# Kernel tuning notes

Measured on AMD Instinct MI355X. Metric: run time of the kernel, lower is better.

## Reference

```python
import jax, jax.numpy as jnp
import numpy as np

N_NODES = 500_000
N_EDGES = 16_000_000
N_COLORS = 64


def _mix(v, c1, c2):
    """32-bit integer hash (lowbias32-style avalanche mix)."""
    v = v.astype(jnp.uint32)
    v = (v ^ (v >> 16)) * jnp.uint32(c1)
    v = (v ^ (v >> 13)) * jnp.uint32(c2)
    return v ^ (v >> 16)


def setup_inputs() -> dict:
    key = jax.random.key(0)
    k1, k2 = jax.random.split(key)
    x = jax.random.randint(k1, (N_NODES,), 0, N_COLORS, dtype=jnp.int32)
    edge_index = jax.random.randint(k2, (2, N_EDGES), 0, N_NODES, dtype=jnp.int32)
    return {"x": x, "edge_index": edge_index}


def reference(x, edge_index):
    """One Weisfeiler-Lehman color-refinement step.

    Faithful semantics of WLConvOptimized.forward: each node's new label is
    determined by the equivalence class of (own label, multiset of incoming
    neighbor labels). Instead of Python tuple-sort + hash()+dict, we use a
    permutation-invariant multiset hash (sum of two independent 32-bit hashes
    of neighbor labels, combined with the node's own label hash) and then a
    sort-based dense relabeling. Nodes get equal output labels iff their
    (label, neighbor-multiset) signatures collide -- same partition as the
    original (up to astronomically unlikely hash collisions); label numbering
    is canonical (sorted-signature order) rather than dict-insertion order.
    """
    num_nodes = x.shape[0]
    row, col = edge_index[0], edge_index[1]  # message flows row (src) -> col (dst)

    # two independent per-label hashes
    ha = _mix(x, 0x045D9F3B, 0x045D9F3B)
    hb = _mix(x, 0x9E3779B1, 0x85EBCA77)

    # permutation-invariant multiset hash of incoming neighbor labels (gather + scatter-add)
    sum_a = jnp.zeros(num_nodes, jnp.uint32).at[col].add(ha[row])
    sum_b = jnp.zeros(num_nodes, jnp.uint32).at[col].add(hb[row])

    # combine own label with neighbor multiset, re-avalanche
    sig_a = _mix(ha * jnp.uint32(0x27D4EB2F) + sum_a, 0xC2B2AE3D, 0x165667B1)
    sig_b = _mix(hb * jnp.uint32(0x61C88647) + sum_b, 0x045D9F3B, 0x27D4EB2F)

    # dense relabel: sort by (sig_a, sig_b), number distinct signatures 0..K-1
    order = jnp.lexsort((sig_b, sig_a))
    sa, sb = sig_a[order], sig_b[order]
    new_grp = jnp.concatenate([
        jnp.zeros(1, jnp.int32),
        ((sa[1:] != sa[:-1]) | (sb[1:] != sb[:-1])).astype(jnp.int32),
    ])
    labels_sorted = jnp.cumsum(new_grp).astype(jnp.int32)
    out = jnp.zeros(num_nodes, jnp.int32).at[order].set(labels_sorted)
    return out
```

## Files before the change

### kernel.cpp

```cpp
#include <hip/hip_runtime.h>
#include <stdint.h>

#define LOG_B 17
#define NB (1u << LOG_B)
#define FINE_NODES 1024
#define NBKT 512
#define CSH 10
#define EPB 16384
#define ITERS (EPB / 4 / 256)

__host__ __device__ constexpr uint32_t cmix(uint32_t v, uint32_t c1, uint32_t c2) {
    v = (v ^ (v >> 16)) * c1;
    v = (v ^ (v >> 13)) * c2;
    return v ^ (v >> 16);
}

__device__ __forceinline__ uint32_t mixh(uint32_t v, uint32_t c1, uint32_t c2) {
    v = (v ^ (v >> 16)) * c1;
    v = (v ^ (v >> 13)) * c2;
    return v ^ (v >> 16);
}

struct Luts { uint32_t ha[64]; uint32_t hb[64]; };
constexpr Luts make_luts() {
    Luts l{};
    for (uint32_t i = 0; i < 64; i++) {
        l.ha[i] = cmix(i, 0x045D9F3Bu, 0x045D9F3Bu);
        l.hb[i] = cmix(i, 0x9E3779B1u, 0x85EBCA77u);
    }
    return l;
}
__constant__ Luts LUT = make_luts();

__global__ __launch_bounds__(256) void k_pre(const int4* __restrict__ x4,
                                             uchar4* __restrict__ xc4, int n4) {
    int i = blockIdx.x * 256 + threadIdx.x;
    if (i >= n4) return;
    int4 v = x4[i];
    xc4[i] = make_uchar4((uint8_t)v.x, (uint8_t)v.y, (uint8_t)v.z, (uint8_t)v.w);
}

__global__ __launch_bounds__(256, 4) void k_bin(const int* __restrict__ row, const int* __restrict__ col,
                                                const uint8_t* __restrict__ xc, uint16_t* __restrict__ bins,
                                                uint32_t* __restrict__ cursor, int E, int cap) {
    __shared__ uint16_t stage[EPB];
    __shared__ uint32_t hist[NBKT];
    __shared__ uint16_t gb16[NBKT];
    __shared__ uint32_t wsum[4];
    int t = threadIdx.x;
    int lane = t & 63, wid = t >> 6;
    int base = blockIdx.x * EPB;
    int nend = min(E - base, EPB);
    for (int b = t; b < NBKT; b += 256) hist[b] = 0;
    __syncthreads();

    const int4* col4 = (const int4*)(col + base);
    const int4* row4 = (const int4*)(row + base);

    bool fast = (nend == EPB);
    uint32_t rec[ITERS * 4];

    if (fast) {
#pragma unroll
        for (int it = 0; it < ITERS; ++it) {
            int k = t + it * 256;
            int4 c = col4[k];
            int4 r = row4[k];
            atomicAdd(&hist[(uint32_t)c.x >> CSH], 1u);
            atomicAdd(&hist[(uint32_t)c.y >> CSH], 1u);
            atomicAdd(&hist[(uint32_t)c.z >> CSH], 1u);
            atomicAdd(&hist[(uint32_t)c.w >> CSH], 1u);
            rec[it * 4 + 0] = ((uint32_t)c.x << 6) | (uint32_t)xc[r.x];
            rec[it * 4 + 1] = ((uint32_t)c.y << 6) | (uint32_t)xc[r.y];
            rec[it * 4 + 2] = ((uint32_t)c.z << 6) | (uint32_t)xc[r.z];
            rec[it * 4 + 3] = ((uint32_t)c.w << 6) | (uint32_t)xc[r.w];
        }
    } else {
        int n4 = nend >> 2;
        for (int k = t; k < n4; k += 256) {
            int4 c = col4[k];
            atomicAdd(&hist[(uint32_t)c.x >> CSH], 1u);
            atomicAdd(&hist[(uint32_t)c.y >> CSH], 1u);
            atomicAdd(&hist[(uint32_t)c.z >> CSH], 1u);
            atomicAdd(&hist[(uint32_t)c.w >> CSH], 1u);
        }
        for (int k = (n4 << 2) + t; k < nend; k += 256)
            atomicAdd(&hist[(uint32_t)col[base + k] >> CSH], 1u);
    }
    __syncthreads();

    int b0 = 2 * t;
    uint32_t h0 = hist[b0], h1 = hist[b0 + 1];
    uint32_t s = h0 + h1;
    uint32_t inc = s;
    for (int off = 1; off < 64; off <<= 1) {
        uint32_t nv = __shfl_up(inc, (unsigned)off, 64);
        if (lane >= off) inc += nv;
    }
    if (lane == 63) wsum[wid] = inc;
    __syncthreads();
    uint32_t woff = 0;
    for (int w = 0; w < wid; w++) woff += wsum[w];
    uint32_t e0 = woff + inc - s;
    uint32_t g0 = h0 ? atomicAdd(&cursor[b0], h0) : 0u;
    uint32_t g1 = h1 ? atomicAdd(&cursor[b0 + 1], h1) : 0u;
    gb16[b0] = (uint16_t)g0;
    gb16[b0 + 1] = (uint16_t)g1;
    hist[b0] = e0 << 16;
    hist[b0 + 1] = (e0 + h0) << 16;
    __syncthreads();

    if (fast) {
#pragma unroll
        for (int it = 0; it < ITERS * 4; ++it) {
            uint32_t rv = rec[it];
            uint32_t b = rv >> 16;
            uint32_t o = atomicAdd(&hist[b], 1u);
            stage[(o >> 16) + (o & 0xFFFFu)] = (uint16_t)rv;
        }
    } else {
        int n4 = nend >> 2;
        for (int k = t; k < n4; k += 256) {
            int4 c = col4[k];
            int4 r = row4[k];
            {
                uint32_t d = (uint32_t)c.x, b = d >> CSH;
                uint32_t o = atomicAdd(&hist[b], 1u);
                stage[(o >> 16) + (o & 0xFFFFu)] = (uint16_t)(((d & 1023u) << 6) | (uint32_t)xc[r.x]);
            }
            {
                uint32_t d = (uint32_t)c.y, b = d >> CSH;
                uint32_t o = atomicAdd(&hist[b], 1u);
                stage[(o >> 16) + (o & 0xFFFFu)] = (uint16_t)(((d & 1023u) << 6) | (uint32_t)xc[r.y]);
            }
            {
                uint32_t d = (uint32_t)c.z, b = d >> CSH;
                uint32_t o = atomicAdd(&hist[b], 1u);
                stage[(o >> 16) + (o & 0xFFFFu)] = (uint16_t)(((d & 1023u) << 6) | (uint32_t)xc[r.z]);
            }
            {
                uint32_t d = (uint32_t)c.w, b = d >> CSH;
                uint32_t o = atomicAdd(&hist[b], 1u);
                stage[(o >> 16) + (o & 0xFFFFu)] = (uint16_t)(((d & 1023u) << 6) | (uint32_t)xc[r.w]);
            }
        }
        for (int k = (n4 << 2) + t; k < nend; k += 256) {
            int i = base + k;
            uint32_t d = (uint32_t)col[i], b = d >> CSH;
            uint32_t o = atomicAdd(&hist[b], 1u);
            stage[(o >> 16) + (o & 0xFFFFu)] = (uint16_t)(((d & 1023u) << 6) | (uint32_t)xc[row[i]]);
        }
    }
    __syncthreads();

    int sub = lane >> 4, l16 = lane & 15;
    for (int b = wid * 4 + sub; b < NBKT; b += 16) {
        uint32_t hv = hist[b];
        uint32_t cnt = hv & 0xFFFFu;
        if (!cnt) continue;
        uint32_t s0 = hv >> 16;
        uint16_t* dst = bins + (size_t)b * (uint32_t)cap + gb16[b];
        for (uint32_t off = l16; off < cnt; off += 16)
            dst[off] = stage[s0 + off];
    }
}

__global__ __launch_bounds__(1024) void k_accsig(const uint16_t* __restrict__ bins,
                                                 const uint32_t* __restrict__ cursor,
                                                 const uint8_t* __restrict__ xc,
                                                 unsigned long long* __restrict__ sigs,
                                                 uint32_t* __restrict__ bcnt, int N, int cap) {
    __shared__ uint32_t sA[FINE_NODES];
    __shared__ uint32_t sB[FINE_NODES];
    __shared__ uint32_t lA[64], lB[64];
    int t = threadIdx.x;
    int b = blockIdx.x;
    sA[t] = 0;
    sB[t] = 0;
    if (t < 64) { lA[t] = LUT.ha[t]; lB[t] = LUT.hb[t]; }
    __syncthreads();

    uint32_t m = cursor[b];
    const uint16_t* mybins = bins + (size_t)b * (uint32_t)cap;
    const uint2* p16v = (const uint2*)mybins;
    uint32_t m4 = m >> 2;
    for (uint32_t k = t; k < m4; k += 1024) {
        uint2 rv = p16v[k];
        {
            uint32_t rec = rv.x & 0xFFFFu, n = rec >> 6, c = rec & 63u;
            atomicAdd(&sA[n], lA[c]);
            atomicAdd(&sB[n], lB[c]);
        }
        {
            uint32_t rec = rv.x >> 16, n = rec >> 6, c = rec & 63u;
            atomicAdd(&sA[n], lA[c]);
            atomicAdd(&sB[n], lB[c]);
        }
        {
            uint32_t rec = rv.y & 0xFFFFu, n = rec >> 6, c = rec & 63u;
            atomicAdd(&sA[n], lA[c]);
            atomicAdd(&sB[n], lB[c]);
        }
        {
            uint32_t rec = rv.y >> 16, n = rec >> 6, c = rec & 63u;
            atomicAdd(&sA[n], lA[c]);
            atomicAdd(&sB[n], lB[c]);
        }
    }
    for (uint32_t k = (m4 << 2) + t; k < m; k += 1024) {
        uint32_t rec = mybins[k], n = rec >> 6, c = rec & 63u;
        atomicAdd(&sA[n], lA[c]);
        atomicAdd(&sB[n], lB[c]);
    }
    __syncthreads();

    int g = b * FINE_NODES + t;
    if (g < N) {
        uint32_t xv = (uint32_t)xc[g];
        uint32_t ha = lA[xv];
        uint32_t hb = lB[xv];
        uint32_t sa = mixh(ha * 0x27D4EB2Fu + sA[t], 0xC2B2AE3Du, 0x165667B1u);
        uint32_t sb = mixh(hb * 0x61C88647u + sB[t], 0x045D9F3Bu, 0x27D4EB2Fu);
        unsigned long long key = ((unsigned long long)sa << 32) | (unsigned long long)sb;
        sigs[g] = key;
        atomicAdd(&bcnt[(uint32_t)(key >> (64 - LOG_B))], 1u);
    }
}

__global__ __launch_bounds__(256) void k_scan1(const uint32_t* __restrict__ in,
                                               uint32_t* __restrict__ out,
                                               uint32_t* __restrict__ part) {
    __shared__ uint32_t wsum[4];
    int t = threadIdx.x;
    int lane = t & 63, wid = t >> 6;
    int base = blockIdx.x * 1024 + 4 * t;
    uint4 v = *(const uint4*)(in + base);
    uint32_t s = v.x + v.y + v.z + v.w;
    uint32_t inc = s;
    for (int off = 1; off < 64; off <<= 1) {
        uint32_t nv = __shfl_up(inc, (unsigned)off, 64);
        if (lane >= off) inc += nv;
    }
    if (lane == 63) wsum[wid] = inc;
    __syncthreads();
    uint32_t woff = 0;
    for (int w = 0; w < wid; w++) woff += wsum[w];
    uint32_t e = woff + inc - s;
    uint4 o;
    o.x = e; o.y = e + v.x; o.z = o.y + v.y; o.w = o.z + v.z;
    *(uint4*)(out + base) = o;
    if (t == 255) part[blockIdx.x] = wsum[0] + wsum[1] + wsum[2] + wsum[3];
}

__global__ void k_scan2(uint32_t* __restrict__ part) {
    __shared__ uint32_t s[256];
    int t = threadIdx.x;
    uint32_t v = part[t];
    s[t] = v;
    __syncthreads();
    for (int off = 1; off < 256; off <<= 1) {
        uint32_t add = (t >= off) ? s[t - off] : 0u;
        __syncthreads();
        s[t] += add;
        __syncthreads();
    }
    part[t] = s[t] - v;
}

__global__ __launch_bounds__(256) void k_scan3(uint32_t* __restrict__ out,
                                               const uint32_t* __restrict__ part) {
    int base = blockIdx.x * 1024 + 4 * threadIdx.x;
    uint32_t p = part[blockIdx.x];
    uint4 v = *(const uint4*)(out + base);
    v.x += p; v.y += p; v.z += p; v.w += p;
    *(uint4*)(out + base) = v;
}

__global__ void k_scatter(const unsigned long long* __restrict__ sigs,
                          const uint32_t* __restrict__ boff, uint32_t* __restrict__ bcur,
                          unsigned long long* __restrict__ skey, uint32_t* __restrict__ snode,
                          int N) {
    int i = blockIdx.x * blockDim.x + threadIdx.x;
    if (i >= N) return;
    unsigned long long key = sigs[i];
    uint32_t b = (uint32_t)(key >> (64 - LOG_B));
    uint32_t pos = boff[b] + atomicAdd(&bcur[b], 1u);
    skey[pos] = key;
    snode[pos] = (uint32_t)i;
}

__global__ void k_bsort(unsigned long long* __restrict__ skey, uint32_t* __restrict__ snode,
                        const uint32_t* __restrict__ boff, uint32_t* __restrict__ ldx,
                        uint32_t* __restrict__ dcnt, int N) {
    int b = blockIdx.x * blockDim.x + threadIdx.x;
    if (b >= (int)NB) return;
    uint32_t s0 = boff[b];
    uint32_t s1 = (b == (int)NB - 1) ? (uint32_t)N : boff[b + 1];
    for (uint32_t i = s0 + 1; i < s1; i++) {
        unsigned long long k = skey[i];
        uint32_t nd = snode[i];
        uint32_t j = i;
        while (j > s0 && skey[j - 1] > k) {
            skey[j] = skey[j - 1];
            snode[j] = snode[j - 1];
            j--;
        }
        skey[j] = k;
        snode[j] = nd;
    }
    uint32_t d = 0;
    unsigned long long prev = 0ull;
    for (uint32_t i = s0; i < s1; i++) {
        unsigned long long k = skey[i];
        if (i == s0 || k != prev) d++;
        prev = k;
        ldx[i] = d - 1;
    }
    dcnt[b] = d;
}

__global__ void k_out(const unsigned long long* __restrict__ skey,
                      const uint32_t* __restrict__ snode, const uint32_t* __restrict__ ldx,
                      const uint32_t* __restrict__ doff, int* __restrict__ out, int N) {
    int i = blockIdx.x * blockDim.x + threadIdx.x;
    if (i >= N) return;
    unsigned long long key = skey[i];
    uint32_t b = (uint32_t)(key >> (64 - LOG_B));
    out[snode[i]] = (int)(doff[b] + ldx[i]);
}

extern "C" void kernel_launch(void* const* d_in, const int* in_sizes, int n_in,
                              void* d_out, int out_size, void* d_ws, size_t ws_size,
                              hipStream_t stream) {
    const int* x = (const int*)d_in[0];
    const int* ei = (const int*)d_in[1];
    int N = in_sizes[0];
    int E = in_sizes[1] / 2;
    const int* row = ei;
    const int* col = ei + E;

    int nacc = (N + FINE_NODES - 1) / FINE_NODES;
    int cap = E / NBKT + (E / NBKT) / 16 + 1024;
    cap = (cap + 3) & ~3;

    char* p = (char*)d_ws;
    auto alloc = [&](size_t bytes) -> char* {
        char* r = p;
        p += (bytes + 255) & ~(size_t)255;
        return r;
    };
    uint32_t* cursor = (uint32_t*)alloc((size_t)NBKT * 4);
    uint32_t* bcnt   = (uint32_t*)alloc((size_t)NB * 4);
    uint32_t* bcur   = (uint32_t*)alloc((size_t)NB * 4);
    uint32_t* dcnt   = (uint32_t*)alloc((size_t)NB * 4);
    uint32_t* part   = (uint32_t*)alloc(256 * 4);
    size_t zbytes = (size_t)(p - (char*)d_ws);
    uint8_t* xc = (uint8_t*)alloc((size_t)N);
    unsigned long long* sigs = (unsigned long long*)alloc((size_t)N * 8);
    uint16_t* bins = (uint16_t*)alloc((size_t)NBKT * cap * 2);
    char* q = (char*)bins;
    auto alias = [&](size_t bytes) -> char* {
        char* r = q;
        q += (bytes + 255) & ~(size_t)255;
        return r;
    };
    unsigned long long* skey = (unsigned long long*)alias((size_t)N * 8);
    uint32_t* snode = (uint32_t*)alias((size_t)N * 4);
    uint32_t* ldx   = (uint32_t*)alias((size_t)N * 4);
    uint32_t* boff  = (uint32_t*)alias((size_t)NB * 4);
    uint32_t* doff  = (uint32_t*)alias((size_t)NB * 4);

    hipMemsetAsync(d_ws, 0, zbytes, stream);

    int nbN = (N + 255) / 256;
    int nbBin = (E + EPB - 1) / EPB;
    int n4 = N / 4;

    k_pre<<<(n4 + 255) / 256, 256, 0, stream>>>((const int4*)x, (uchar4*)xc, n4);
    k_bin<<<nbBin, 256, 0, stream>>>(row, col, xc, bins, cursor, E, cap);
    k_accsig<<<nacc, 1024, 0, stream>>>(bins, cursor, xc, sigs, bcnt, N, cap);

    k_scan1<<<NB / 1024, 256, 0, stream>>>(bcnt, boff, part);
    k_scan2<<<1, 256, 0, stream>>>(part);
    k_scan3<<<NB / 1024, 256, 0, stream>>>(boff, part);

    k_scatter<<<nbN, 256, 0, stream>>>(sigs, boff, bcur, skey, snode, N);
    k_bsort<<<NB / 256, 256, 0, stream>>>(skey, snode, boff, ldx, dcnt, N);

    k_scan1<<<NB / 1024, 256, 0, stream>>>(dcnt, doff, part);
    k_scan2<<<1, 256, 0, stream>>>(part);
    k_scan3<<<NB / 1024, 256, 0, stream>>>(doff, part);

    k_out<<<nbN, 256, 0, stream>>>(skey, snode, ldx, doff, (int*)d_out, N);
}
```

Measured before the change: 397.9 us.

## Fuse scan, scatter, bucket sort and output into one cooperative kernel

Replaces the chain of eight small kernels (two three-pass scans, scatter, bucket sort, output) with a single cooperative kernel of 512 blocks that uses grid-wide syncs between phases. This is meant to remove per-launch overhead and the idle gaps between dependent launches in the tail. The cost is many grid.sync barriers, a cooperative-launch residency requirement, and one block doing the partial-sum scan serially while the other blocks wait.

```diff
diff --git a/kernel.cpp b/kernel.cpp
--- a/kernel.cpp
+++ b/kernel.cpp
@@ -1,5 +1,8 @@
 #include <hip/hip_runtime.h>
+#include <hip/hip_cooperative_groups.h>
 #include <stdint.h>
+
+namespace cg = cooperative_groups;
 
 #define LOG_B 17
 #define NB (1u << LOG_B)
@@ -227,106 +230,110 @@
     }
 }
 
-__global__ __launch_bounds__(256) void k_scan1(const uint32_t* __restrict__ in,
-                                               uint32_t* __restrict__ out,
-                                               uint32_t* __restrict__ part) {
-    __shared__ uint32_t wsum[4];
+
+__device__ __forceinline__ void scan_nb(const uint32_t* __restrict__ in,
+                                        uint32_t* __restrict__ outp,
+                                        uint32_t* __restrict__ part,
+                                        uint32_t* sh, uint32_t* shw,
+                                        cg::grid_group& grid) {
     int t = threadIdx.x;
     int lane = t & 63, wid = t >> 6;
-    int base = blockIdx.x * 1024 + 4 * t;
-    uint4 v = *(const uint4*)(in + base);
-    uint32_t s = v.x + v.y + v.z + v.w;
-    uint32_t inc = s;
+    int g = blockIdx.x * 256 + t;
+    uint32_t v = in[g];
+    uint32_t inc = v;
     for (int off = 1; off < 64; off <<= 1) {
         uint32_t nv = __shfl_up(inc, (unsigned)off, 64);
         if (lane >= off) inc += nv;
     }
-    if (lane == 63) wsum[wid] = inc;
+    if (lane == 63) shw[wid] = inc;
     __syncthreads();
     uint32_t woff = 0;
-    for (int w = 0; w < wid; w++) woff += wsum[w];
-    uint32_t e = woff + inc - s;
-    uint4 o;
-    o.x = e; o.y = e + v.x; o.z = o.y + v.y; o.w = o.z + v.z;
-    *(uint4*)(out + base) = o;
-    if (t == 255) part[blockIdx.x] = wsum[0] + wsum[1] + wsum[2] + wsum[3];
-}
-
-__global__ void k_scan2(uint32_t* __restrict__ part) {
-    __shared__ uint32_t s[256];
+    for (int w = 0; w < wid; w++) woff += shw[w];
+    uint32_t excl = woff + inc - v;
+    if (t == 255) part[blockIdx.x] = woff + inc;
+    grid.sync();
+    if (blockIdx.x == 0) {
+        uint32_t o0 = part[t], o1 = part[t + 256];
+        sh[t] = o0; sh[t + 256] = o1;
+        __syncthreads();
+        for (int off = 1; off < 512; off <<= 1) {
+            uint32_t a0 = (t >= off) ? sh[t - off] : 0u;
+            uint32_t a1 = (t + 256 >= off) ? sh[t + 256 - off] : 0u;
+            __syncthreads();
+            sh[t] += a0; sh[t + 256] += a1;
+            __syncthreads();
+        }
+        part[t] = sh[t] - o0;
+        part[t + 256] = sh[t + 256] - o1;
+    }
+    grid.sync();
+    outp[g] = excl + part[blockIdx.x];
+}
+
+__global__ __launch_bounds__(256) void k_tail(const unsigned long long* __restrict__ sigs,
+                                              const uint32_t* __restrict__ bcnt,
+                                              uint32_t* __restrict__ boff,
+                                              uint32_t* __restrict__ bcur,
+                                              unsigned long long* __restrict__ skey,
+                                              uint32_t* __restrict__ snode,
+                                              uint32_t* __restrict__ ldx,
+                                              uint32_t* __restrict__ dcnt,
+                                              uint32_t* __restrict__ doff,
+                                              uint32_t* __restrict__ part,
+                                              int* __restrict__ out, int N) {
+    cg::grid_group grid = cg::this_grid();
+    __shared__ uint32_t sh[512];
+    __shared__ uint32_t shw[4];
     int t = threadIdx.x;
-    uint32_t v = part[t];
-    s[t] = v;
-    __syncthreads();
-    for (int off = 1; off < 256; off <<= 1) {
-        uint32_t add = (t >= off) ? s[t - off] : 0u;
-        __syncthreads();
-        s[t] += add;
-        __syncthreads();
-    }
-    part[t] = s[t] - v;
-}
-
-__global__ __launch_bounds__(256) void k_scan3(uint32_t* __restrict__ out,
-                                               const uint32_t* __restrict__ part) {
-    int base = blockIdx.x * 1024 + 4 * threadIdx.x;
-    uint32_t p = part[blockIdx.x];
-    uint4 v = *(const uint4*)(out + base);
-    v.x += p; v.y += p; v.z += p; v.w += p;
-    *(uint4*)(out + base) = v;
-}
-
-__global__ void k_scatter(const unsigned long long* __restrict__ sigs,
-                          const uint32_t* __restrict__ boff, uint32_t* __restrict__ bcur,
-                          unsigned long long* __restrict__ skey, uint32_t* __restrict__ snode,
-                          int N) {
-    int i = blockIdx.x * blockDim.x + threadIdx.x;
-    if (i >= N) return;
-    unsigned long long key = sigs[i];
-    uint32_t b = (uint32_t)(key >> (64 - LOG_B));
-    uint32_t pos = boff[b] + atomicAdd(&bcur[b], 1u);
-    skey[pos] = key;
-    snode[pos] = (uint32_t)i;
-}
-
-__global__ void k_bsort(unsigned long long* __restrict__ skey, uint32_t* __restrict__ snode,
-                        const uint32_t* __restrict__ boff, uint32_t* __restrict__ ldx,
-                        uint32_t* __restrict__ dcnt, int N) {
-    int b = blockIdx.x * blockDim.x + threadIdx.x;
-    if (b >= (int)NB) return;
-    uint32_t s0 = boff[b];
-    uint32_t s1 = (b == (int)NB - 1) ? (uint32_t)N : boff[b + 1];
-    for (uint32_t i = s0 + 1; i < s1; i++) {
-        unsigned long long k = skey[i];
-        uint32_t nd = snode[i];
-        uint32_t j = i;
-        while (j > s0 && skey[j - 1] > k) {
-            skey[j] = skey[j - 1];
-            snode[j] = snode[j - 1];
-            j--;
-        }
-        skey[j] = k;
-        snode[j] = nd;
-    }
-    uint32_t d = 0;
-    unsigned long long prev = 0ull;
-    for (uint32_t i = s0; i < s1; i++) {
-        unsigned long long k = skey[i];
-        if (i == s0 || k != prev) d++;
-        prev = k;
-        ldx[i] = d - 1;
-    }
-    dcnt[b] = d;
-}
-
-__global__ void k_out(const unsigned long long* __restrict__ skey,
-                      const uint32_t* __restrict__ snode, const uint32_t* __restrict__ ldx,
-                      const uint32_t* __restrict__ doff, int* __restrict__ out, int N) {
-    int i = blockIdx.x * blockDim.x + threadIdx.x;
-    if (i >= N) return;
-    unsigned long long key = skey[i];
-    uint32_t b = (uint32_t)(key >> (64 - LOG_B));
-    out[snode[i]] = (int)(doff[b] + ldx[i]);
+    int g = blockIdx.x * 256 + t;
+
+    scan_nb(bcnt, boff, part, sh, shw, grid);
+    grid.sync();
+
+    for (int i = g; i < N; i += (int)NB) {
+        unsigned long long key = sigs[i];
+        uint32_t b = (uint32_t)(key >> (64 - LOG_B));
+        uint32_t pos = boff[b] + atomicAdd(&bcur[b], 1u);
+        skey[pos] = key;
+        snode[pos] = (uint32_t)i;
+    }
+    grid.sync();
+
+    {
+        uint32_t s0 = boff[g];
+        uint32_t s1 = (g == (int)NB - 1) ? (uint32_t)N : boff[g + 1];
+        for (uint32_t i = s0 + 1; i < s1; i++) {
+            unsigned long long k = skey[i];
+            uint32_t nd = snode[i];
+            uint32_t j = i;
+            while (j > s0 && skey[j - 1] > k) {
+                skey[j] = skey[j - 1];
+                snode[j] = snode[j - 1];
+                j--;
+            }
+            skey[j] = k;
+            snode[j] = nd;
+        }
+        uint32_t d = 0;
+        unsigned long long prev = 0ull;
+        for (uint32_t i = s0; i < s1; i++) {
+            unsigned long long k = skey[i];
+            if (i == s0 || k != prev) d++;
+            prev = k;
+            ldx[i] = d - 1;
+        }
+        dcnt[g] = d;
+    }
+    grid.sync();
+
+    scan_nb(dcnt, doff, part, sh, shw, grid);
+    grid.sync();
+
+    for (int i = g; i < N; i += (int)NB) {
+        unsigned long long key = skey[i];
+        uint32_t b = (uint32_t)(key >> (64 - LOG_B));
+        out[snode[i]] = (int)(doff[b] + ldx[i]);
+    }
 }
 
 extern "C" void kernel_launch(void* const* d_in, const int* in_sizes, int n_in,
@@ -353,7 +360,7 @@
     uint32_t* bcnt   = (uint32_t*)alloc((size_t)NB * 4);
     uint32_t* bcur   = (uint32_t*)alloc((size_t)NB * 4);
     uint32_t* dcnt   = (uint32_t*)alloc((size_t)NB * 4);
-    uint32_t* part   = (uint32_t*)alloc(256 * 4);
+    uint32_t* part   = (uint32_t*)alloc(512 * 4);
     size_t zbytes = (size_t)(p - (char*)d_ws);
     uint8_t* xc = (uint8_t*)alloc((size_t)N);
     unsigned long long* sigs = (unsigned long long*)alloc((size_t)N * 8);
@@ -372,7 +379,6 @@
 
     hipMemsetAsync(d_ws, 0, zbytes, stream);
 
-    int nbN = (N + 255) / 256;
     int nbBin = (E + EPB - 1) / EPB;
     int n4 = N / 4;
 
@@ -380,16 +386,10 @@
     k_bin<<<nbBin, 256, 0, stream>>>(row, col, xc, bins, cursor, E, cap);
     k_accsig<<<nacc, 1024, 0, stream>>>(bins, cursor, xc, sigs, bcnt, N, cap);
 
-    k_scan1<<<NB / 1024, 256, 0, stream>>>(bcnt, boff, part);
-    k_scan2<<<1, 256, 0, stream>>>(part);
-    k_scan3<<<NB / 1024, 256, 0, stream>>>(boff, part);
-
-    k_scatter<<<nbN, 256, 0, stream>>>(sigs, boff, bcur, skey, snode, N);
-    k_bsort<<<NB / 256, 256, 0, stream>>>(skey, snode, boff, ldx, dcnt, N);
-
-    k_scan1<<<NB / 1024, 256, 0, stream>>>(dcnt, doff, part);
-    k_scan2<<<1, 256, 0, stream>>>(part);
-    k_scan3<<<NB / 1024, 256, 0, stream>>>(doff, part);
-
-    k_out<<<nbN, 256, 0, stream>>>(skey, snode, ldx, doff, (int*)d_out, N);
-}
+    int* outp = (int*)d_out;
+    void* args[] = { (void*)&sigs, (void*)&bcnt, (void*)&boff, (void*)&bcur,
+                     (void*)&skey, (void*)&snode, (void*)&ldx, (void*)&dcnt,
+                     (void*)&doff, (void*)&part, (void*)&outp, (void*)&N };
+    hipLaunchCooperativeKernel((const void*)k_tail, dim3(NB / 256), dim3(256),
+                               args, 0, stream);
+}
```

New measurement: 835.5 us. 110% more time.

## Fuse bucket sort, distinct-count scan and output scatter into one decoupled-lookback kernel

Applied to the files above, without the earlier changes.

Replaces the per-bucket insertion sort, the three-kernel distinct-count scan and the output kernel with a single k_rank kernel. Each block loads its 256 buckets' keys into LDS and sorts them there, keeping a 16-bit permutation instead of moving node ids in global memory. Block totals are combined with a decoupled look-back prefix, and output labels are written directly. This removes four launches and several global round-trips (ldx, doff, dcnt). In exchange it relies on forward-progress spinning across blocks and falls back to global-memory sorting when a block's range exceeds the LDS capacity.

```diff
diff --git a/kernel.cpp b/kernel.cpp
--- a/kernel.cpp
+++ b/kernel.cpp
@@ -8,6 +8,7 @@
 #define CSH 10
 #define EPB 16384
 #define ITERS (EPB / 4 / 256)
+#define RCAP 1536
 
 __host__ __device__ constexpr uint32_t cmix(uint32_t v, uint32_t c1, uint32_t c2) {
     v = (v ^ (v >> 16)) * c1;
@@ -289,44 +290,151 @@
     snode[pos] = (uint32_t)i;
 }
 
-__global__ void k_bsort(unsigned long long* __restrict__ skey, uint32_t* __restrict__ snode,
-                        const uint32_t* __restrict__ boff, uint32_t* __restrict__ ldx,
-                        uint32_t* __restrict__ dcnt, int N) {
-    int b = blockIdx.x * blockDim.x + threadIdx.x;
-    if (b >= (int)NB) return;
+__device__ __forceinline__ uint32_t lb_prefix(unsigned long long* agg, int bid, int lane) {
+    uint32_t prefix = 0;
+    int base = bid - 1;
+    for (;;) {
+        int idx = base - lane;
+        unsigned long long v;
+        if (idx >= 0) {
+            do {
+                v = __hip_atomic_load(&agg[idx], __ATOMIC_ACQUIRE, __HIP_MEMORY_SCOPE_AGENT);
+            } while ((v >> 32) == 0ull);
+        } else {
+            v = (2ull << 32);
+        }
+        bool incl = (v >> 32) == 2ull;
+        unsigned long long mask = __ballot(incl);
+        int fl = mask ? (__ffsll(mask) - 1) : 64;
+        uint32_t contrib = (lane <= fl) ? (uint32_t)v : 0u;
+        for (int off = 32; off; off >>= 1) contrib += __shfl_down(contrib, off, 64);
+        contrib = __shfl(contrib, 0, 64);
+        prefix += contrib;
+        if (fl < 64) return prefix;
+        base -= 64;
+    }
+}
+
+__global__ __launch_bounds__(256) void k_rank(const uint32_t* __restrict__ boff,
+                                              unsigned long long* __restrict__ skey,
+                                              uint32_t* __restrict__ snode,
+                                              unsigned long long* __restrict__ aggD,
+                                              int* __restrict__ out, int N) {
+    __shared__ unsigned long long lkey[RCAP];
+    __shared__ uint16_t perm[RCAP];
+    __shared__ uint32_t shw[4];
+    __shared__ uint32_t sh_tot;
+    __shared__ uint32_t sh_pref;
+    __shared__ int sh_ovf;
+    int t = threadIdx.x;
+    int lane = t & 63, wid = t >> 6;
+    int bid = blockIdx.x;
+    int B0 = bid * 256;
+    int b = B0 + t;
+    uint32_t E0 = boff[B0];
+    uint32_t E1 = (B0 + 256 >= (int)NB) ? (uint32_t)N : boff[B0 + 256];
+    uint32_t cnt = E1 - E0;
     uint32_t s0 = boff[b];
     uint32_t s1 = (b == (int)NB - 1) ? (uint32_t)N : boff[b + 1];
-    for (uint32_t i = s0 + 1; i < s1; i++) {
-        unsigned long long k = skey[i];
-        uint32_t nd = snode[i];
-        uint32_t j = i;
-        while (j > s0 && skey[j - 1] > k) {
-            skey[j] = skey[j - 1];
-            snode[j] = snode[j - 1];
-            j--;
-        }
-        skey[j] = k;
-        snode[j] = nd;
-    }
+    if (t == 0) { sh_ovf = (cnt > RCAP); sh_pref = 0; }
+    __syncthreads();
+    bool ovf = (sh_ovf != 0);
+
+    if (!ovf) {
+        for (uint32_t i = t; i < cnt; i += 256) { lkey[i] = skey[E0 + i]; perm[i] = (uint16_t)i; }
+        __syncthreads();
+        uint32_t l0 = s0 - E0, l1 = s1 - E0;
+        for (uint32_t i = l0 + 1; i < l1; i++) {
+            unsigned long long k = lkey[i];
+            uint16_t p = perm[i];
+            uint32_t j = i;
+            while (j > l0 && lkey[j - 1] > k) {
+                lkey[j] = lkey[j - 1];
+                perm[j] = perm[j - 1];
+                j--;
+            }
+            lkey[j] = k;
+            perm[j] = p;
+        }
+    } else {
+        for (uint32_t i = s0 + 1; i < s1; i++) {
+            unsigned long long k = skey[i];
+            uint32_t nd = snode[i];
+            uint32_t j = i;
+            while (j > s0 && skey[j - 1] > k) {
+                skey[j] = skey[j - 1];
+                snode[j] = snode[j - 1];
+                j--;
+            }
+            skey[j] = k;
+            snode[j] = nd;
+        }
+    }
+
     uint32_t d = 0;
     unsigned long long prev = 0ull;
-    for (uint32_t i = s0; i < s1; i++) {
-        unsigned long long k = skey[i];
-        if (i == s0 || k != prev) d++;
-        prev = k;
-        ldx[i] = d - 1;
-    }
-    dcnt[b] = d;
-}
-
-__global__ void k_out(const unsigned long long* __restrict__ skey,
-                      const uint32_t* __restrict__ snode, const uint32_t* __restrict__ ldx,
-                      const uint32_t* __restrict__ doff, int* __restrict__ out, int N) {
-    int i = blockIdx.x * blockDim.x + threadIdx.x;
-    if (i >= N) return;
-    unsigned long long key = skey[i];
-    uint32_t b = (uint32_t)(key >> (64 - LOG_B));
-    out[snode[i]] = (int)(doff[b] + ldx[i]);
+    if (!ovf) {
+        uint32_t l0 = s0 - E0, l1 = s1 - E0;
+        for (uint32_t i = l0; i < l1; i++) {
+            unsigned long long k = lkey[i];
+            if (i == l0 || k != prev) d++;
+            prev = k;
+        }
+    } else {
+        for (uint32_t i = s0; i < s1; i++) {
+            unsigned long long k = skey[i];
+            if (i == s0 || k != prev) d++;
+            prev = k;
+        }
+    }
+
+    uint32_t inc = d;
+    for (int off = 1; off < 64; off <<= 1) {
+        uint32_t nv = __shfl_up(inc, (unsigned)off, 64);
+        if (lane >= off) inc += nv;
+    }
+    if (lane == 63) shw[wid] = inc;
+    __syncthreads();
+    uint32_t woff = 0;
+    for (int w = 0; w < wid; w++) woff += shw[w];
+    uint32_t dexcl = woff + inc - d;
+    if (t == 255) sh_tot = woff + inc;
+    __syncthreads();
+
+    if (wid == 0) {
+        uint32_t blk_total = sh_tot;
+        if (t == 0)
+            __hip_atomic_store(&aggD[bid], (1ull << 32) | (unsigned long long)blk_total,
+                               __ATOMIC_RELEASE, __HIP_MEMORY_SCOPE_AGENT);
+        uint32_t pref = 0;
+        if (bid > 0) pref = lb_prefix(aggD, bid, lane);
+        if (t == 0) {
+            __hip_atomic_store(&aggD[bid], (2ull << 32) | (unsigned long long)(blk_total + pref),
+                               __ATOMIC_RELEASE, __HIP_MEMORY_SCOPE_AGENT);
+            sh_pref = pref;
+        }
+    }
+    __syncthreads();
+    uint32_t D0 = sh_pref;
+
+    d = 0;
+    prev = 0ull;
+    if (!ovf) {
+        uint32_t l0 = s0 - E0, l1 = s1 - E0;
+        for (uint32_t i = l0; i < l1; i++) {
+            unsigned long long k = lkey[i];
+            if (i == l0 || k != prev) d++;
+            prev = k;
+            out[snode[E0 + (uint32_t)perm[i]]] = (int)(D0 + dexcl + d - 1);
+        }
+    } else {
+        for (uint32_t i = s0; i < s1; i++) {
+            unsigned long long k = skey[i];
+            if (i == s0 || k != prev) d++;
+            prev = k;
+            out[snode[i]] = (int)(D0 + dexcl + d - 1);
+        }
+    }
 }
 
 extern "C" void kernel_launch(void* const* d_in, const int* in_sizes, int n_in,
@@ -352,8 +460,8 @@
     uint32_t* cursor = (uint32_t*)alloc((size_t)NBKT * 4);
     uint32_t* bcnt   = (uint32_t*)alloc((size_t)NB * 4);
     uint32_t* bcur   = (uint32_t*)alloc((size_t)NB * 4);
-    uint32_t* dcnt   = (uint32_t*)alloc((size_t)NB * 4);
     uint32_t* part   = (uint32_t*)alloc(256 * 4);
+    unsigned long long* aggD = (unsigned long long*)alloc((size_t)(NB / 256) * 8);
     size_t zbytes = (size_t)(p - (char*)d_ws);
     uint8_t* xc = (uint8_t*)alloc((size_t)N);
     unsigned long long* sigs = (unsigned long long*)alloc((size_t)N * 8);
@@ -366,9 +474,7 @@
     };
     unsigned long long* skey = (unsigned long long*)alias((size_t)N * 8);
     uint32_t* snode = (uint32_t*)alias((size_t)N * 4);
-    uint32_t* ldx   = (uint32_t*)alias((size_t)N * 4);
     uint32_t* boff  = (uint32_t*)alias((size_t)NB * 4);
-    uint32_t* doff  = (uint32_t*)alias((size_t)NB * 4);
 
     hipMemsetAsync(d_ws, 0, zbytes, stream);
 
@@ -385,11 +491,5 @@
     k_scan3<<<NB / 1024, 256, 0, stream>>>(boff, part);
 
     k_scatter<<<nbN, 256, 0, stream>>>(sigs, boff, bcur, skey, snode, N);
-    k_bsort<<<NB / 256, 256, 0, stream>>>(skey, snode, boff, ldx, dcnt, N);
-
-    k_scan1<<<NB / 1024, 256, 0, stream>>>(dcnt, doff, part);
-    k_scan2<<<1, 256, 0, stream>>>(part);
-    k_scan3<<<NB / 1024, 256, 0, stream>>>(doff, part);
-
-    k_out<<<nbN, 256, 0, stream>>>(skey, snode, ldx, doff, (int*)d_out, N);
-}
+    k_rank<<<NB / 256, 256, 0, stream>>>(boff, skey, snode, aggD, (int*)d_out, N);
+}
```

Measured after the change: 408.1 us. 1.03x slower.

## Fuse scans with decoupled look-back and drop node-index payload from bucket sort

Applied to the files above, without the earlier changes.

Replaces each three-kernel scan with a single-pass decoupled look-back scan, and folds the distinct-count scan into the bucket sort kernel. The node-index array and per-element local index are removed. The output kernel instead re-finds each node's key by walking its sorted bucket. This cuts kernel launches and memory traffic, at the cost of spin-waiting across blocks and a short per-node search in the output pass.

```diff
diff --git a/kernel.cpp b/kernel.cpp
--- a/kernel.cpp
+++ b/kernel.cpp
@@ -8,6 +8,8 @@
 #define CSH 10
 #define EPB 16384
 #define ITERS (EPB / 4 / 256)
+
+typedef unsigned long long ull;
 
 __host__ __device__ constexpr uint32_t cmix(uint32_t v, uint32_t c1, uint32_t c2) {
     v = (v ^ (v >> 16)) * c1;
@@ -168,7 +170,7 @@
 __global__ __launch_bounds__(1024) void k_accsig(const uint16_t* __restrict__ bins,
                                                  const uint32_t* __restrict__ cursor,
                                                  const uint8_t* __restrict__ xc,
-                                                 unsigned long long* __restrict__ sigs,
+                                                 ull* __restrict__ sigs,
                                                  uint32_t* __restrict__ bcnt, int N, int cap) {
     __shared__ uint32_t sA[FINE_NODES];
     __shared__ uint32_t sB[FINE_NODES];
@@ -221,19 +223,46 @@
         uint32_t hb = lB[xv];
         uint32_t sa = mixh(ha * 0x27D4EB2Fu + sA[t], 0xC2B2AE3Du, 0x165667B1u);
         uint32_t sb = mixh(hb * 0x61C88647u + sB[t], 0x045D9F3Bu, 0x27D4EB2Fu);
-        unsigned long long key = ((unsigned long long)sa << 32) | (unsigned long long)sb;
+        ull key = ((ull)sa << 32) | (ull)sb;
         sigs[g] = key;
         atomicAdd(&bcnt[(uint32_t)(key >> (64 - LOG_B))], 1u);
     }
 }
 
-__global__ __launch_bounds__(256) void k_scan1(const uint32_t* __restrict__ in,
-                                               uint32_t* __restrict__ out,
-                                               uint32_t* __restrict__ part) {
+__device__ __forceinline__ uint32_t lb_prefix(ull* agg, int bid, int lane) {
+    uint32_t prefix = 0;
+    int base = bid - 1;
+    for (;;) {
+        int idx = base - lane;
+        ull v;
+        if (idx >= 0) {
+            do {
+                v = __hip_atomic_load(&agg[idx], __ATOMIC_ACQUIRE, __HIP_MEMORY_SCOPE_AGENT);
+            } while ((v >> 32) == 0ull);
+        } else {
+            v = (2ull << 32);
+        }
+        bool incl = (v >> 32) == 2ull;
+        ull mask = __ballot(incl);
+        int fl = mask ? (__ffsll(mask) - 1) : 64;
+        uint32_t contrib = (lane <= fl) ? (uint32_t)v : 0u;
+        for (int off = 32; off; off >>= 1) contrib += __shfl_down(contrib, off, 64);
+        contrib = __shfl(contrib, 0, 64);
+        prefix += contrib;
+        if (fl < 64) return prefix;
+        base -= 64;
+    }
+}
+
+__global__ __launch_bounds__(256) void k_scanlb(const uint32_t* __restrict__ in,
+                                                uint32_t* __restrict__ out,
+                                                ull* __restrict__ agg) {
     __shared__ uint32_t wsum[4];
+    __shared__ uint32_t sh_pref;
     int t = threadIdx.x;
     int lane = t & 63, wid = t >> 6;
-    int base = blockIdx.x * 1024 + 4 * t;
+    int bid = blockIdx.x;
+    int base = bid * 1024 + 4 * t;
     uint4 v = *(const uint4*)(in + base);
     uint32_t s = v.x + v.y + v.z + v.w;
     uint32_t inc = s;
@@ -246,87 +275,113 @@
     uint32_t woff = 0;
     for (int w = 0; w < wid; w++) woff += wsum[w];
     uint32_t e = woff + inc - s;
+    uint32_t tot = wsum[0] + wsum[1] + wsum[2] + wsum[3];
+    if (wid == 0) {
+        if (t == 0)
+            __hip_atomic_store(&agg[bid], (1ull << 32) | (ull)tot,
+                               __ATOMIC_RELEASE, __HIP_MEMORY_SCOPE_AGENT);
+        uint32_t pref = 0;
+        if (bid > 0) pref = lb_prefix(agg, bid, lane);
+        if (t == 0) {
+            __hip_atomic_store(&agg[bid], (2ull << 32) | (ull)(tot + pref),
+                               __ATOMIC_RELEASE, __HIP_MEMORY_SCOPE_AGENT);
+            sh_pref = pref;
+        }
+    }
+    __syncthreads();
+    uint32_t p = sh_pref;
     uint4 o;
-    o.x = e; o.y = e + v.x; o.z = o.y + v.y; o.w = o.z + v.z;
+    o.x = e + p; o.y = o.x + v.x; o.z = o.y + v.y; o.w = o.z + v.z;
     *(uint4*)(out + base) = o;
-    if (t == 255) part[blockIdx.x] = wsum[0] + wsum[1] + wsum[2] + wsum[3];
-}
-
-__global__ void k_scan2(uint32_t* __restrict__ part) {
-    __shared__ uint32_t s[256];
-    int t = threadIdx.x;
-    uint32_t v = part[t];
-    s[t] = v;
-    __syncthreads();
-    for (int off = 1; off < 256; off <<= 1) {
-        uint32_t add = (t >= off) ? s[t - off] : 0u;
-        __syncthreads();
-        s[t] += add;
-        __syncthreads();
-    }
-    part[t] = s[t] - v;
-}
-
-__global__ __launch_bounds__(256) void k_scan3(uint32_t* __restrict__ out,
-                                               const uint32_t* __restrict__ part) {
-    int base = blockIdx.x * 1024 + 4 * threadIdx.x;
-    uint32_t p = part[blockIdx.x];
-    uint4 v = *(const uint4*)(out + base);
-    v.x += p; v.y += p; v.z += p; v.w += p;
-    *(uint4*)(out + base) = v;
-}
-
-__global__ void k_scatter(const unsigned long long* __restrict__ sigs,
+}
+
+__global__ void k_scatter(const ull* __restrict__ sigs,
                           const uint32_t* __restrict__ boff, uint32_t* __restrict__ bcur,
-                          unsigned long long* __restrict__ skey, uint32_t* __restrict__ snode,
-                          int N) {
+                          ull* __restrict__ skey, int N) {
     int i = blockIdx.x * blockDim.x + threadIdx.x;
     if (i >= N) return;
-    unsigned long long key = sigs[i];
+    ull key = sigs[i];
     uint32_t b = (uint32_t)(key >> (64 - LOG_B));
     uint32_t pos = boff[b] + atomicAdd(&bcur[b], 1u);
     skey[pos] = key;
-    snode[pos] = (uint32_t)i;
-}
-
-__global__ void k_bsort(unsigned long long* __restrict__ skey, uint32_t* __restrict__ snode,
-                        const uint32_t* __restrict__ boff, uint32_t* __restrict__ ldx,
-                        uint32_t* __restrict__ dcnt, int N) {
-    int b = blockIdx.x * blockDim.x + threadIdx.x;
-    if (b >= (int)NB) return;
+}
+
+__global__ __launch_bounds__(256) void k_bsort2(ull* __restrict__ skey,
+                                                const uint32_t* __restrict__ boff,
+                                                uint32_t* __restrict__ rbase,
+                                                ull* __restrict__ agg, int N) {
+    __shared__ uint32_t wsum[4];
+    __shared__ uint32_t sh_pref;
+    int t = threadIdx.x;
+    int lane = t & 63, wid = t >> 6;
+    int bid = blockIdx.x;
+    int b = bid * 256 + t;
     uint32_t s0 = boff[b];
     uint32_t s1 = (b == (int)NB - 1) ? (uint32_t)N : boff[b + 1];
     for (uint32_t i = s0 + 1; i < s1; i++) {
-        unsigned long long k = skey[i];
-        uint32_t nd = snode[i];
+        ull k = skey[i];
         uint32_t j = i;
         while (j > s0 && skey[j - 1] > k) {
             skey[j] = skey[j - 1];
-            snode[j] = snode[j - 1];
             j--;
         }
         skey[j] = k;
-        snode[j] = nd;
     }
     uint32_t d = 0;
-    unsigned long long prev = 0ull;
+    ull prev = 0ull;
     for (uint32_t i = s0; i < s1; i++) {
-        unsigned long long k = skey[i];
+        ull k = skey[i];
         if (i == s0 || k != prev) d++;
         prev = k;
-        ldx[i] = d - 1;
-    }
-    dcnt[b] = d;
-}
-
-__global__ void k_out(const unsigned long long* __restrict__ skey,
-                      const uint32_t* __restrict__ snode, const uint32_t* __restrict__ ldx,
-                      const uint32_t* __restrict__ doff, int* __restrict__ out, int N) {
-    int i = blockIdx.x * blockDim.x + threadIdx.x;
+    }
+    uint32_t inc = d;
+    for (int off = 1; off < 64; off <<= 1) {
+        uint32_t nv = __shfl_up(inc, (unsigned)off, 64);
+        if (lane >= off) inc += nv;
+    }
+    if (lane == 63) wsum[wid] = inc;
+    __syncthreads();
+    uint32_t woff = 0;
+    for (int w = 0; w < wid; w++) woff += wsum[w];
+    uint32_t dexcl = woff + inc - d;
+    uint32_t tot = wsum[0] + wsum[1] + wsum[2] + wsum[3];
+    if (wid == 0) {
+        if (t == 0)
+            __hip_atomic_store(&agg[bid], (1ull << 32) | (ull)tot,
+                               __ATOMIC_RELEASE, __HIP_MEMORY_SCOPE_AGENT);
+        uint32_t pref = 0;
+        if (bid > 0) pref = lb_prefix(agg, bid, lane);
+        if (t == 0) {
+            __hip_atomic_store(&agg[bid], (2ull << 32) | (ull)(tot + pref),
+                               __ATOMIC_RELEASE, __HIP_MEMORY_SCOPE_AGENT);
+            sh_pref = pref;
+        }
+    }
+    __syncthreads();
+    rbase[b] = sh_pref + dexcl;
+}
+
+__global__ __launch_bounds__(256) void k_out2(const ull* __restrict__ sigs,
+                                              const uint32_t* __restrict__ boff,
+                                              const ull* __restrict__ skey,
+                                              const uint32_t* __restrict__ rbase,
+                                              int* __restrict__ out, int N) {
+    int i = blockIdx.x * 256 + threadIdx.x;
     if (i >= N) return;
-    unsigned long long key = skey[i];
+    ull key = sigs[i];
     uint32_t b = (uint32_t)(key >> (64 - LOG_B));
-    out[snode[i]] = (int)(doff[b] + ldx[i]);
+    uint32_t s0 = boff[b];
+    uint32_t d = 0;
+    ull prev = 0ull;
+    uint32_t j = s0;
+    for (;;) {
+        ull k = skey[j];
+        if (j == s0 || k != prev) d++;
+        if (k == key) break;
+        prev = k;
+        j++;
+    }
+    out[i] = (int)(rbase[b] + d - 1);
 }
 
 extern "C" void kernel_launch(void* const* d_in, const int* in_sizes, int n_in,
@@ -352,11 +407,11 @@
     uint32_t* cursor = (uint32_t*)alloc((size_t)NBKT * 4);
     uint32_t* bcnt   = (uint32_t*)alloc((size_t)NB * 4);
     uint32_t* bcur   = (uint32_t*)alloc((size_t)NB * 4);
-    uint32_t* dcnt   = (uint32_t*)alloc((size_t)NB * 4);
-    uint32_t* part   = (uint32_t*)alloc(256 * 4);
+    ull* aggB = (ull*)alloc((size_t)(NB / 1024) * 8);
+    ull* aggD = (ull*)alloc((size_t)(NB / 256) * 8);
     size_t zbytes = (size_t)(p - (char*)d_ws);
     uint8_t* xc = (uint8_t*)alloc((size_t)N);
-    unsigned long long* sigs = (unsigned long long*)alloc((size_t)N * 8);
+    ull* sigs = (ull*)alloc((size_t)N * 8);
     uint16_t* bins = (uint16_t*)alloc((size_t)NBKT * cap * 2);
     char* q = (char*)bins;
     auto alias = [&](size_t bytes) -> char* {
@@ -364,11 +419,9 @@
         q += (bytes + 255) & ~(size_t)255;
         return r;
     };
-    unsigned long long* skey = (unsigned long long*)alias((size_t)N * 8);
-    uint32_t* snode = (uint32_t*)alias((size_t)N * 4);
-    uint32_t* ldx   = (uint32_t*)alias((size_t)N * 4);
+    ull* skey       = (ull*)alias((size_t)N * 8);
     uint32_t* boff  = (uint32_t*)alias((size_t)NB * 4);
-    uint32_t* doff  = (uint32_t*)alias((size_t)NB * 4);
+    uint32_t* rbase = (uint32_t*)alias((size_t)NB * 4);
 
     hipMemsetAsync(d_ws, 0, zbytes, stream);
 
@@ -380,16 +433,8 @@
     k_bin<<<nbBin, 256, 0, stream>>>(row, col, xc, bins, cursor, E, cap);
     k_accsig<<<nacc, 1024, 0, stream>>>(bins, cursor, xc, sigs, bcnt, N, cap);
 
-    k_scan1<<<NB / 1024, 256, 0, stream>>>(bcnt, boff, part);
-    k_scan2<<<1, 256, 0, stream>>>(part);
-    k_scan3<<<NB / 1024, 256, 0, stream>>>(boff, part);
-
-    k_scatter<<<nbN, 256, 0, stream>>>(sigs, boff, bcur, skey, snode, N);
-    k_bsort<<<NB / 256, 256, 0, stream>>>(skey, snode, boff, ldx, dcnt, N);
-
-    k_scan1<<<NB / 1024, 256, 0, stream>>>(dcnt, doff, part);
-    k_scan2<<<1, 256, 0, stream>>>(part);
-    k_scan3<<<NB / 1024, 256, 0, stream>>>(doff, part);
-
-    k_out<<<nbN, 256, 0, stream>>>(skey, snode, ldx, doff, (int*)d_out, N);
-}
+    k_scanlb<<<NB / 1024, 256, 0, stream>>>(bcnt, boff, aggB);
+    k_scatter<<<nbN, 256, 0, stream>>>(sigs, boff, bcur, skey, N);
+    k_bsort2<<<NB / 256, 256, 0, stream>>>(skey, boff, rbase, aggD, N);
+    k_out2<<<nbN, 256, 0, stream>>>(sigs, boff, skey, rbase, (int*)d_out, N);
+}
```

Result: slower. 492.0 us (+23.7%).
